# Kernel tuning notes

Hardware: AMD Instinct MI355X
Metric: run time of the kernel (lower is better)

The kernel has to match this reference:

```python
import jax, jax.numpy as jnp
import numpy as np

B, C, S, NSEG = 8, 64, 64, 256   # batch, channels, spatial, superpixel classes
DIM, DEPTH, HEADS, DH, MLP, NCLS = 256, 4, 8, 64, 1024, 4
D2 = 2 * DIM                      # transformer width = 512
INNER = HEADS * DH                # 512


def layernorm(x, g, b, eps=1e-5):
    mu = jnp.mean(x, axis=-1, keepdims=True)
    var = jnp.var(x, axis=-1, keepdims=True)
    return (x - mu) * jax.lax.rsqrt(var + eps) * g + b


def setup_inputs() -> dict:
    key = jax.random.key(0)
    ks = jax.random.split(key, 16)
    inp = {
        "image": jax.random.normal(ks[0], (B, 3, S, S), jnp.float32),
        "feature": jax.random.normal(ks[1], (3, B, C, S, S), jnp.float32),
        "superpixel": jax.random.randint(ks[2], (B, S, S), 0, NSEG),
        # patch embedding Linear(64*64*64 -> dim)
        "W_patch": jax.random.normal(ks[3], (C * S * S, DIM), jnp.float32) * (C * S * S) ** -0.5,
        "b_patch": jnp.zeros((DIM,), jnp.float32),
        # per-layer stacked params (depth leading axis)
        "ln1_g": jnp.ones((DEPTH, D2), jnp.float32),
        "ln1_b": jnp.zeros((DEPTH, D2), jnp.float32),
        "Wqkv": jax.random.normal(ks[4], (DEPTH, D2, 3 * INNER), jnp.float32) * D2 ** -0.5,
        "Wo": jax.random.normal(ks[5], (DEPTH, INNER, D2), jnp.float32) * INNER ** -0.5,
        "bo": jnp.zeros((DEPTH, D2), jnp.float32),
        "ln2_g": jnp.ones((DEPTH, D2), jnp.float32),
        "ln2_b": jnp.zeros((DEPTH, D2), jnp.float32),
        "W1": jax.random.normal(ks[6], (DEPTH, D2, MLP), jnp.float32) * D2 ** -0.5,
        "b1": jnp.zeros((DEPTH, MLP), jnp.float32),
        "W2": jax.random.normal(ks[7], (DEPTH, MLP, D2), jnp.float32) * MLP ** -0.5,
        "b2": jnp.zeros((DEPTH, D2), jnp.float32),
        # mlp_head: LayerNorm(2*dim) + Linear(2*dim, num_classes)
        "lnf_g": jnp.ones((D2,), jnp.float32),
        "lnf_b": jnp.zeros((D2,), jnp.float32),
        "W_head": jax.random.normal(ks[8], (D2, NCLS), jnp.float32) * D2 ** -0.5,
        "b_head": jnp.zeros((NCLS,), jnp.float32),
    }
    return inp


def _forward(image, feature, superpixel,
             W_patch, b_patch,
             ln1_g, ln1_b, Wqkv, Wo, bo, ln2_g, ln2_b, W1, b1, W2, b2,
             lnf_g, lnf_b, W_head, b_head):
    feat2 = feature[2]                                   # [B,C,S,S]
    # Fuse (one-hot mask * feature) -> flatten(b j h) -> Linear into a
    # per-pixel projection followed by a segment-sum over superpixel ids.
    Wr = W_patch.reshape(C, S, S, DIM)                   # matches (b j h) flatten order
    T = jnp.einsum('ibjh,bjhd->ijhd', feat2, Wr)         # [B,S,S,DIM]
    onehot = jax.nn.one_hot(superpixel, NSEG, dtype=T.dtype)  # [B,S,S,NSEG]
    x = jnp.einsum('ijha,ijhd->iad', onehot, T) + b_patch     # [B,NSEG,DIM]

    local = x
    g = jnp.max(x, axis=1, keepdims=True)                # global max over patches
    x = jnp.concatenate([jnp.broadcast_to(g, local.shape), local], axis=2)  # [B,256,2*dim]

    scale = DH ** -0.5
    for d in range(DEPTH):
        # attention block (pre-norm, residual)
        h = layernorm(x, ln1_g[d], ln1_b[d])
        qkv = h @ Wqkv[d]                                # [B,N,3*inner]
        q, k, v = jnp.split(qkv, 3, axis=-1)
        q = q.reshape(*q.shape[:2], HEADS, DH).transpose(0, 2, 1, 3)
        k = k.reshape(*k.shape[:2], HEADS, DH).transpose(0, 2, 1, 3)
        v = v.reshape(*v.shape[:2], HEADS, DH).transpose(0, 2, 1, 3)
        dots = jnp.einsum('bhnd,bhmd->bhnm', q, k) * scale
        attn = jax.nn.softmax(dots, axis=-1)
        o = jnp.einsum('bhnm,bhmd->bhnd', attn, v)
        o = o.transpose(0, 2, 1, 3).reshape(*x.shape[:2], INNER)
        x = x + (o @ Wo[d] + bo[d])
        # feedforward block (GELU exact, as nn.GELU default)
        h = layernorm(x, ln2_g[d], ln2_b[d])
        h = jax.nn.gelu(h @ W1[d] + b1[d], approximate=False)
        x = x + (h @ W2[d] + b2[d])

    return layernorm(x, lnf_g, lnf_b) @ W_head + b_head  # [B,256,num_classes]


def reference(image, feature, superpixel,
              W_patch, b_patch,
              ln1_g, ln1_b, Wqkv, Wo, bo, ln2_g, ln2_b, W1, b1, W2, b2,
              lnf_g, lnf_b, W_head, b_head):
    return _forward(image, feature, superpixel,
                    W_patch, b_patch,
                    ln1_g, ln1_b, Wqkv, Wo, bo, ln2_g, ln2_b, W1, b1, W2, b2,
                    lnf_g, lnf_b, W_head, b_head)
```

## Files before the change

### kernel.cpp

```cpp
#include <hip/hip_runtime.h>
#include <hip/hip_bf16.h>
#include <math.h>

#define NB 8
#define NC 64
#define NS 64
#define NPIX 4096
#define NSEG 256
#define DIM 256
#define DEPTH 4
#define HEADS 8
#define DHD 64
#define MLPD 1024
#define NCLS 4
#define D2 512
#define INNER 512
#define NTOK 2048

typedef unsigned short u16;
typedef unsigned int u32;
typedef __attribute__((ext_vector_type(4))) float f32x4;
typedef __attribute__((ext_vector_type(8))) short short8;

__device__ __forceinline__ u16 bf16_rne(float x) {
    u32 u = __float_as_uint(x);
    return (u16)((u + 0x7FFFu + ((u >> 16) & 1u)) >> 16);
}
__device__ __forceinline__ void split2(float x, u16& h, u16& l) {
    h = bf16_rne(x);
    float hf = __uint_as_float((u32)h << 16);
    l = bf16_rne(x - hf);
}

__global__ __launch_bounds__(256) void k_init_x0(float* __restrict__ x0,
                                                 const float* __restrict__ bp) {
    int idx = blockIdx.x * 256 + threadIdx.x;
    x0[idx] = bp[idx & (DIM - 1)];
}

#define PPB 4
__global__ __launch_bounds__(256) void k_patch(const float* __restrict__ feature,
                                               const int* __restrict__ sp,
                                               const float* __restrict__ Wp,
                                               float* __restrict__ x0) {
    __shared__ __align__(16) float f[NB * NC][PPB];
    __shared__ int seg[NB][PPB];
    const int p0 = blockIdx.x * PPB;
    const int t = threadIdx.x;
    const float* feat2 = feature + (size_t)2 * NB * NC * NPIX;
    #pragma unroll
    for (int i = 0; i < 2; ++i) {
        int pair = t + i * 256;
        *(float4*)&f[pair][0] = *(const float4*)&feat2[(size_t)pair * NPIX + p0];
    }
    if (t < NB * PPB) seg[t >> 2][t & 3] = sp[(t >> 2) * NPIX + p0 + (t & 3)];
    __syncthreads();
    const int d = t;
    for (int q = 0; q < PPB; ++q) {
        float acc[NB];
        #pragma unroll
        for (int b = 0; b < NB; ++b) acc[b] = 0.f;
        const float* wcol = Wp + (size_t)(p0 + q) * DIM + d;
        #pragma unroll 8
        for (int c = 0; c < NC; ++c) {
            float w = wcol[(size_t)c * NPIX * DIM];
            #pragma unroll
            for (int b = 0; b < NB; ++b) acc[b] = fmaf(f[b * NC + c][q], w, acc[b]);
        }
        #pragma unroll
        for (int b = 0; b < NB; ++b)
            atomicAdd(&x0[((b * NSEG) + seg[b][q]) * DIM + d], acc[b]);
    }
}

__global__ __launch_bounds__(256) void k_concat(const float* __restrict__ x0,
                                                float* __restrict__ x) {
    const int b = blockIdx.x, part = blockIdx.y;
    const int d = threadIdx.x;
    const float* xb = x0 + (size_t)b * NSEG * DIM;
    float g = -INFINITY;
    for (int s = 0; s < NSEG; ++s) g = fmaxf(g, xb[s * DIM + d]);
    for (int s = part * 16; s < part * 16 + 16; ++s) {
        float* row = x + ((size_t)(b * NSEG + s)) * D2;
        row[d] = g;
        row[DIM + d] = xb[s * DIM + d];
    }
}

__global__ __launch_bounds__(128) void k_ln(const float* __restrict__ x,
                                            const float* __restrict__ g,
                                            const float* __restrict__ bta,
                                            u16* __restrict__ outH,
                                            u16* __restrict__ outL) {
    const int row = blockIdx.x, t = threadIdx.x;
    const float4 v = *(const float4*)(x + (size_t)row * D2 + t * 4);
    float s = v.x + v.y + v.z + v.w;
    float ss = v.x * v.x + v.y * v.y + v.z * v.z + v.w * v.w;
    #pragma unroll
    for (int o = 32; o; o >>= 1) { s += __shfl_down(s, o); ss += __shfl_down(ss, o); }
    __shared__ float red[4];
    if ((t & 63) == 0) { red[(t >> 6) * 2] = s; red[(t >> 6) * 2 + 1] = ss; }
    __syncthreads();
    s = red[0] + red[2]; ss = red[1] + red[3];
    const float mu = s * (1.f / D2);
    const float rstd = rsqrtf(ss * (1.f / D2) - mu * mu + 1e-5f);
    const float4 g4 = *(const float4*)(g + t * 4);
    const float4 b4 = *(const float4*)(bta + t * 4);
    float o4[4] = {(v.x - mu) * rstd * g4.x + b4.x,
                   (v.y - mu) * rstd * g4.y + b4.y,
                   (v.z - mu) * rstd * g4.z + b4.z,
                   (v.w - mu) * rstd * g4.w + b4.w};
    u16 h[4], l[4];
    #pragma unroll
    for (int i = 0; i < 4; ++i) split2(o4[i], h[i], l[i]);
    *(ushort4*)(outH + (size_t)row * D2 + t * 4) = make_ushort4(h[0], h[1], h[2], h[3]);
    *(ushort4*)(outL + (size_t)row * D2 + t * 4) = make_ushort4(l[0], l[1], l[2], l[3]);
}

__device__ __forceinline__ void cvt_tile(const float* __restrict__ src, int K, int N,
                                         u16* __restrict__ dH, u16* __restrict__ dL,
                                         int k0, int n0) {
    __shared__ __align__(16) float ls[32][33];
    const int t = threadIdx.x;
    const int r = t >> 3, cg = t & 7;
    const float4 v = *(const float4*)(src + (size_t)(k0 + r) * N + n0 + cg * 4);
    ls[r][cg * 4 + 0] = v.x; ls[r][cg * 4 + 1] = v.y;
    ls[r][cg * 4 + 2] = v.z; ls[r][cg * 4 + 3] = v.w;
    __syncthreads();
    u16 h[4], l[4];
    #pragma unroll
    for (int i = 0; i < 4; ++i) split2(ls[cg * 4 + i][r], h[i], l[i]);
    *(ushort4*)(dH + (size_t)(n0 + r) * K + k0 + cg * 4) = make_ushort4(h[0], h[1], h[2], h[3]);
    *(ushort4*)(dL + (size_t)(n0 + r) * K + k0 + cg * 4) = make_ushort4(l[0], l[1], l[2], l[3]);
}

__global__ __launch_bounds__(256) void k_cvtT(const float* __restrict__ src,
                                              u16* __restrict__ dH, u16* __restrict__ dL,
                                              int K, int N) {
    cvt_tile(src, K, N, dH, dL, blockIdx.x * 32, blockIdx.y * 32);
}

__global__ __launch_bounds__(256) void k_cvtT3(const float* __restrict__ sO,
                                               const float* __restrict__ s1,
                                               const float* __restrict__ s2,
                                               u16* __restrict__ wb) {
    int K, N; const float* src; u16 *dH, *dL;
    if (blockIdx.z == 0)      { K = 512;  N = 512;  src = sO; dH = wb;           dL = wb + 262144; }
    else if (blockIdx.z == 1) { K = 512;  N = 1024; src = s1; dH = wb + 524288;  dL = wb + 1048576; }
    else                      { K = 1024; N = 512;  src = s2; dH = wb + 1572864; dL = wb + 2097152; }
    const int k0 = blockIdx.x * 32, n0 = blockIdx.y * 32;
    if (k0 >= K || n0 >= N) return;
    cvt_tile(src, K, N, dH, dL, k0, n0);
}

template<int K, int NN, int MODE>
__global__ __launch_bounds__(256) void k_mfmm(const u16* __restrict__ Ah,
                                              const u16* __restrict__ Al,
                                              const u16* __restrict__ Bh,
                                              const u16* __restrict__ Bl,
                                              const float* __restrict__ bias,
                                              float* __restrict__ Cf,
                                              u16* __restrict__ CoH,
                                              u16* __restrict__ CoL) {
    __shared__ __align__(16) u16 AsH[128][40], AsL[128][40], BsH[128][40], BsL[128][40];
    const int m0 = blockIdx.x * 128, n0 = blockIdx.y * 128;
    const int t = threadIdx.x;
    const int srow = t >> 1, soff = (t & 1) * 16;
    const int lane = t & 63;
    const int wr = (t >> 7) & 1, wc = (t >> 6) & 1;
    const int lrow = lane & 15, lk = lane >> 4;

    const u16* pAh = Ah + (size_t)(m0 + srow) * K + soff;
    const u16* pAl = Al + (size_t)(m0 + srow) * K + soff;
    const u16* pBh = Bh + (size_t)(n0 + srow) * K + soff;
    const u16* pBl = Bl + (size_t)(n0 + srow) * K + soff;

    uint4 rAh0 = *(const uint4*)pAh,       rAh1 = *(const uint4*)(pAh + 8);
    uint4 rAl0 = *(const uint4*)pAl,       rAl1 = *(const uint4*)(pAl + 8);
    uint4 rBh0 = *(const uint4*)pBh,       rBh1 = *(const uint4*)(pBh + 8);
    uint4 rBl0 = *(const uint4*)pBl,       rBl1 = *(const uint4*)(pBl + 8);

    f32x4 acc[4][4];
    #pragma unroll
    for (int i = 0; i < 4; ++i)
        #pragma unroll
        for (int j = 0; j < 4; ++j) acc[i][j] = (f32x4){0.f, 0.f, 0.f, 0.f};

    #pragma unroll 1
    for (int k0 = 0; k0 < K; k0 += 32) {
        __syncthreads();
        *(uint4*)&AsH[srow][soff] = rAh0;  *(uint4*)&AsH[srow][soff + 8] = rAh1;
        *(uint4*)&AsL[srow][soff] = rAl0;  *(uint4*)&AsL[srow][soff + 8] = rAl1;
        *(uint4*)&BsH[srow][soff] = rBh0;  *(uint4*)&BsH[srow][soff + 8] = rBh1;
        *(uint4*)&BsL[srow][soff] = rBl0;  *(uint4*)&BsL[srow][soff + 8] = rBl1;
        __syncthreads();
        if (k0 + 32 < K) {
            rAh0 = *(const uint4*)(pAh + k0 + 32);  rAh1 = *(const uint4*)(pAh + k0 + 40);
            rAl0 = *(const uint4*)(pAl + k0 + 32);  rAl1 = *(const uint4*)(pAl + k0 + 40);
            rBh0 = *(const uint4*)(pBh + k0 + 32);  rBh1 = *(const uint4*)(pBh + k0 + 40);
            rBl0 = *(const uint4*)(pBl + k0 + 32);  rBl1 = *(const uint4*)(pBl + k0 + 40);
        }
        short8 ah[4], al[4], bh[4], bl[4];
        #pragma unroll
        for (int i = 0; i < 4; ++i) {
            ah[i] = *(const short8*)&AsH[wr * 64 + i * 16 + lrow][lk * 8];
            al[i] = *(const short8*)&AsL[wr * 64 + i * 16 + lrow][lk * 8];
            bh[i] = *(const short8*)&BsH[wc * 64 + i * 16 + lrow][lk * 8];
            bl[i] = *(const short8*)&BsL[wc * 64 + i * 16 + lrow][lk * 8];
        }
        #pragma unroll
        for (int i = 0; i < 4; ++i)
            #pragma unroll
            for (int j = 0; j < 4; ++j) {
                acc[i][j] = __builtin_amdgcn_mfma_f32_16x16x32_bf16(ah[i], bh[j], acc[i][j], 0, 0, 0);
                acc[i][j] = __builtin_amdgcn_mfma_f32_16x16x32_bf16(ah[i], bl[j], acc[i][j], 0, 0, 0);
                acc[i][j] = __builtin_amdgcn_mfma_f32_16x16x32_bf16(al[i], bh[j], acc[i][j], 0, 0, 0);
            }
    }
    #pragma unroll
    for (int i = 0; i < 4; ++i) {
        #pragma unroll
        for (int j = 0; j < 4; ++j) {
            #pragma unroll
            for (int r = 0; r < 4; ++r) {
                const int row = m0 + wr * 64 + i * 16 + lk * 4 + r;
                const int col = n0 + wc * 64 + j * 16 + lrow;
                float v = acc[i][j][r];
                if (MODE == 0) {
                    const int which = col >> 9, hd = (col >> 6) & 7, dh = col & 63;
                    const int b = row >> 8, nn = row & 255;
                    Cf[(size_t)which * (NB * HEADS * NSEG * DHD) +
                       ((size_t)(b * HEADS + hd) * NSEG + nn) * DHD + dh] = v;
                } else if (MODE == 1) {
                    float* xp = Cf + (size_t)row * NN + col;
                    *xp += v + bias[col];
                } else {
                    v += bias[col];
                    float gl = 0.5f * v * (1.f + erff(v * 0.70710678118654752f));
                    u16 h, l; split2(gl, h, l);
                    CoH[(size_t)row * NN + col] = h;
                    CoL[(size_t)row * NN + col] = l;
                }
            }
        }
    }
}

__device__ __forceinline__ void gemm_tile(const float* __restrict__ A, int lda,
                                          const float* __restrict__ Bm, int ldb,
                                          int K, float acc[4][4],
                                          float (*As)[68], float (*Bs)[64]) {
    const int t = threadIdx.x;
    const int arow = t >> 2, akg = t & 3;
    const int bk = t >> 4, bng = t & 15;
    const int tx = t & 15, ty = t >> 4;
    for (int k0 = 0; k0 < K; k0 += 16) {
        const float4 av = *(const float4*)(A + (size_t)arow * lda + k0 + akg * 4);
        const float4 bv = *(const float4*)(Bm + (size_t)(k0 + bk) * ldb + bng * 4);
        __syncthreads();
        As[akg * 4 + 0][arow] = av.x;
        As[akg * 4 + 1][arow] = av.y;
        As[akg * 4 + 2][arow] = av.z;
        As[akg * 4 + 3][arow] = av.w;
        *(float4*)(&Bs[bk][bng * 4]) = bv;
        __syncthreads();
        #pragma unroll
        for (int u = 0; u < 16; ++u) {
            const float4 a4 = *(const float4*)(&As[u][ty * 4]);
            const float4 b4 = *(const float4*)(&Bs[u][tx * 4]);
            const float a[4] = {a4.x, a4.y, a4.z, a4.w};
            const float b[4] = {b4.x, b4.y, b4.z, b4.w};
            #pragma unroll
            for (int i = 0; i < 4; ++i)
                #pragma unroll
                for (int j = 0; j < 4; ++j)
                    acc[i][j] = fmaf(a[i], b[j], acc[i][j]);
        }
    }
}

__global__ __launch_bounds__(256) void k_qk(const float* __restrict__ q,
                                            const float* __restrict__ kmat,
                                            float* __restrict__ sc) {
    __shared__ __align__(16) float Qs[16][68], Ks[16][68];
    const int bh = blockIdx.z;
    const int t = threadIdx.x;
    const int arow = t >> 2, akg = t & 3, tx = t & 15, ty = t >> 4;
    const float* qb = q + ((size_t)bh * NSEG + blockIdx.x * 64) * DHD;
    const float* kb = kmat + ((size_t)bh * NSEG + blockIdx.y * 64) * DHD;
    float acc[4][4] = {};
    for (int k0 = 0; k0 < DHD; k0 += 16) {
        const float4 qv = *(const float4*)(qb + arow * DHD + k0 + akg * 4);
        const float4 kv = *(const float4*)(kb + arow * DHD + k0 + akg * 4);
        __syncthreads();
        Qs[akg * 4 + 0][arow] = qv.x; Qs[akg * 4 + 1][arow] = qv.y;
        Qs[akg * 4 + 2][arow] = qv.z; Qs[akg * 4 + 3][arow] = qv.w;
        Ks[akg * 4 + 0][arow] = kv.x; Ks[akg * 4 + 1][arow] = kv.y;
        Ks[akg * 4 + 2][arow] = kv.z; Ks[akg * 4 + 3][arow] = kv.w;
        __syncthreads();
        #pragma unroll
        for (int u = 0; u < 16; ++u) {
            const float4 a4 = *(const float4*)(&Qs[u][ty * 4]);
            const float4 b4 = *(const float4*)(&Ks[u][tx * 4]);
            const float a[4] = {a4.x, a4.y, a4.z, a4.w};
            const float b[4] = {b4.x, b4.y, b4.z, b4.w};
            #pragma unroll
            for (int i = 0; i < 4; ++i)
                #pragma unroll
                for (int j = 0; j < 4; ++j)
                    acc[i][j] = fmaf(a[i], b[j], acc[i][j]);
        }
    }
    float* sb = sc + (size_t)bh * NSEG * NSEG + (size_t)(blockIdx.x * 64) * NSEG + blockIdx.y * 64;
    #pragma unroll
    for (int i = 0; i < 4; ++i) {
        float4 o4 = make_float4(acc[i][0] * 0.125f, acc[i][1] * 0.125f,
                                acc[i][2] * 0.125f, acc[i][3] * 0.125f);
        *(float4*)(sb + (size_t)(ty * 4 + i) * NSEG + tx * 4) = o4;
    }
}

__global__ __launch_bounds__(256) void k_softmax(float* __restrict__ sc) {
    const int row = blockIdx.x * 4 + (threadIdx.x >> 6);
    const int l = threadIdx.x & 63;
    float* p = sc + (size_t)row * 256 + l * 4;
    float4 v = *(float4*)p;
    float m = fmaxf(fmaxf(v.x, v.y), fmaxf(v.z, v.w));
    #pragma unroll
    for (int o = 32; o; o >>= 1) m = fmaxf(m, __shfl_xor(m, o));
    v.x = __expf(v.x - m); v.y = __expf(v.y - m);
    v.z = __expf(v.z - m); v.w = __expf(v.w - m);
    float s = v.x + v.y + v.z + v.w;
    #pragma unroll
    for (int o = 32; o; o >>= 1) s += __shfl_xor(s, o);
    const float r = 1.f / s;
    v.x *= r; v.y *= r; v.z *= r; v.w *= r;
    *(float4*)p = v;
}

__global__ __launch_bounds__(256) void k_pv(const float* __restrict__ sc,
                                            const float* __restrict__ vmat,
                                            u16* __restrict__ oH,
                                            u16* __restrict__ oL) {
    __shared__ __align__(16) float As[16][68], Bs[16][64];
    const int bh = blockIdx.z;
    const int m0 = blockIdx.x * 64;
    float acc[4][4] = {};
    gemm_tile(sc + (size_t)bh * NSEG * NSEG + (size_t)m0 * NSEG, NSEG,
              vmat + (size_t)bh * NSEG * DHD, DHD, NSEG, acc, As, Bs);
    const int t = threadIdx.x, tx = t & 15, ty = t >> 4;
    #pragma unroll
    for (int i = 0; i < 4; ++i) {
        const size_t idx = (size_t)(bh >> 3) * NSEG * INNER + (bh & 7) * DHD +
                           (size_t)(m0 + ty * 4 + i) * INNER + tx * 4;
        u16 h[4], l[4];
        #pragma unroll
        for (int j = 0; j < 4; ++j) split2(acc[i][j], h[j], l[j]);
        *(ushort4*)(oH + idx) = make_ushort4(h[0], h[1], h[2], h[3]);
        *(ushort4*)(oL + idx) = make_ushort4(l[0], l[1], l[2], l[3]);
    }
}

__global__ __launch_bounds__(128) void k_head(const float* __restrict__ x,
                                              const float* __restrict__ g,
                                              const float* __restrict__ bta,
                                              const float* __restrict__ Wh,
                                              const float* __restrict__ bhd,
                                              float* __restrict__ out) {
    const int row = blockIdx.x, t = threadIdx.x;
    const float4 v = *(const float4*)(x + (size_t)row * D2 + t * 4);
    float s = v.x + v.y + v.z + v.w;
    float ss = v.x * v.x + v.y * v.y + v.z * v.z + v.w * v.w;
    #pragma unroll
    for (int o = 32; o; o >>= 1) { s += __shfl_down(s, o); ss += __shfl_down(ss, o); }
    __shared__ float red[4];
    if ((t & 63) == 0) { red[(t >> 6) * 2] = s; red[(t >> 6) * 2 + 1] = ss; }
    __syncthreads();
    s = red[0] + red[2]; ss = red[1] + red[3];
    const float mu = s * (1.f / D2);
    const float rstd = rsqrtf(ss * (1.f / D2) - mu * mu + 1e-5f);
    const float4 g4 = *(const float4*)(g + t * 4);
    const float4 b4 = *(const float4*)(bta + t * 4);
    const float hv[4] = {(v.x - mu) * rstd * g4.x + b4.x,
                         (v.y - mu) * rstd * g4.y + b4.y,
                         (v.z - mu) * rstd * g4.z + b4.z,
                         (v.w - mu) * rstd * g4.w + b4.w};
    float p[4] = {0, 0, 0, 0};
    #pragma unroll
    for (int i = 0; i < 4; ++i) {
        const float4 w = *(const float4*)(Wh + (size_t)(t * 4 + i) * NCLS);
        p[0] = fmaf(hv[i], w.x, p[0]); p[1] = fmaf(hv[i], w.y, p[1]);
        p[2] = fmaf(hv[i], w.z, p[2]); p[3] = fmaf(hv[i], w.w, p[3]);
    }
    #pragma unroll
    for (int o = 32; o; o >>= 1)
        #pragma unroll
        for (int c2 = 0; c2 < 4; ++c2) p[c2] += __shfl_down(p[c2], o);
    __shared__ float red2[2][4];
    if ((t & 63) == 0) {
        #pragma unroll
        for (int c2 = 0; c2 < 4; ++c2) red2[t >> 6][c2] = p[c2];
    }
    __syncthreads();
    if (t < 4) out[(size_t)row * NCLS + t] = red2[0][t] + red2[1][t] + bhd[t];
}

extern "C" void kernel_launch(void* const* d_in, const int* in_sizes, int n_in,
                              void* d_out, int out_size, void* d_ws, size_t ws_size,
                              hipStream_t stream) {
    const float* feature = (const float*)d_in[1];
    const int*   sp      = (const int*)d_in[2];
    const float* Wp      = (const float*)d_in[3];
    const float* bp      = (const float*)d_in[4];
    const float* ln1g    = (const float*)d_in[5];
    const float* ln1b    = (const float*)d_in[6];
    const float* Wqkv    = (const float*)d_in[7];
    const float* Wo      = (const float*)d_in[8];
    const float* bo      = (const float*)d_in[9];
    const float* ln2g    = (const float*)d_in[10];
    const float* ln2b    = (const float*)d_in[11];
    const float* W1      = (const float*)d_in[12];
    const float* b1      = (const float*)d_in[13];
    const float* W2      = (const float*)d_in[14];
    const float* b2      = (const float*)d_in[15];
    const float* lnfg    = (const float*)d_in[16];
    const float* lnfb    = (const float*)d_in[17];
    const float* Wh      = (const float*)d_in[18];
    const float* bhd     = (const float*)d_in[19];
    float* out = (float*)d_out;
    float* ws  = (float*)d_ws;

    float* x    = ws;
    float* x0   = ws + 1048576;
    u16*   hlnH = (u16*)(ws + 1572864);
    u16*   hlnL = hlnH + 1048576;
    u16*   h1H  = (u16*)(ws + 2621440);
    u16*   h1L  = h1H + 2097152;
    float* qkv  = ws + 4718592;
    float* sc   = ws + 7864320;
    u16*   wbuf = (u16*)sc;
    u16*   oH   = (u16*)(ws + 12058624);
    u16*   oL   = oH + 1048576;

    u16* qh = wbuf;
    u16* ql = wbuf + 786432;
    u16* woh = wbuf;
    u16* wol = wbuf + 262144;
    u16* w1h = wbuf + 524288;
    u16* w1l = wbuf + 1048576;
    u16* w2h = wbuf + 1572864;
    u16* w2l = wbuf + 2097152;

    k_init_x0<<<2048, 256, 0, stream>>>(x0, bp);
    k_patch<<<NPIX / PPB, 256, 0, stream>>>(feature, sp, Wp, x0);
    k_concat<<<dim3(NB, 16), 256, 0, stream>>>(x0, x);

    for (int d = 0; d < DEPTH; ++d) {
        k_cvtT<<<dim3(16, 48), 256, 0, stream>>>(Wqkv + (size_t)d * D2 * 3 * INNER,
                                                 qh, ql, D2, 3 * INNER);
        k_ln<<<NTOK, 128, 0, stream>>>(x, ln1g + d * D2, ln1b + d * D2, hlnH, hlnL);
        k_mfmm<512, 1536, 0><<<dim3(16, 12), 256, 0, stream>>>(
            hlnH, hlnL, qh, ql, nullptr, qkv, nullptr, nullptr);
        k_qk<<<dim3(4, 4, 64), 256, 0, stream>>>(qkv, qkv + 1048576, sc);
        k_softmax<<<4096, 256, 0, stream>>>(sc);
        k_pv<<<dim3(4, 1, 64), 256, 0, stream>>>(sc, qkv + 2097152, oH, oL);
        k_cvtT3<<<dim3(32, 32, 3), 256, 0, stream>>>(Wo + (size_t)d * INNER * D2,
                                                     W1 + (size_t)d * D2 * MLPD,
                                                     W2 + (size_t)d * MLPD * D2, wbuf);
        k_mfmm<512, 512, 1><<<dim3(16, 4), 256, 0, stream>>>(
            oH, oL, woh, wol, bo + d * D2, x, nullptr, nullptr);
        k_ln<<<NTOK, 128, 0, stream>>>(x, ln2g + d * D2, ln2b + d * D2, hlnH, hlnL);
        k_mfmm<512, 1024, 2><<<dim3(16, 8), 256, 0, stream>>>(
            hlnH, hlnL, w1h, w1l, b1 + d * MLPD, nullptr, h1H, h1L);
        k_mfmm<1024, 512, 1><<<dim3(16, 4), 256, 0, stream>>>(
            h1H, h1L, w2h, w2l, b2 + d * D2, x, nullptr, nullptr);
    }
    k_head<<<NTOK, 128, 0, stream>>>(x, lnfg, lnfb, Wh, bhd, out);
}
```

Measured before the change: 1.103 ms.

## Fuse attention QK, softmax and PV into one MFMA kernel with split-bf16 QKV

Replaces the three fp32 SIMT attention kernels (QK scores, softmax, PV) with a single fused kernel using bf16x3 split MFMA. The QKV projection epilogue now writes hi/lo bf16 halves directly, with V stored transposed for the PV MFMA operand. Scores stay in registers, and probabilities pass through per-wave LDS, so the 256x256 score matrix no longer round-trips through global memory. The cost is heavy register pressure (16 score accumulators) and scattered 2-byte global stores in the QKV epilogue.

Result: no change. 1.098 ms (-0.5%).

```diff
diff --git a/kernel.cpp b/kernel.cpp
--- a/kernel.cpp
+++ b/kernel.cpp
@@ -229,8 +229,13 @@
                 if (MODE == 0) {
                     const int which = col >> 9, hd = (col >> 6) & 7, dh = col & 63;
                     const int b = row >> 8, nn = row & 255;
-                    Cf[(size_t)which * (NB * HEADS * NSEG * DHD) +
-                       ((size_t)(b * HEADS + hd) * NSEG + nn) * DHD + dh] = v;
+                    u16 h, l; split2(v, h, l);
+                    size_t off;
+                    if (which == 2)
+                        off = (size_t)4194304 + ((size_t)((b * 8 + hd) * 64 + dh)) * 256 + nn;
+                    else
+                        off = (size_t)which * 2097152 + ((size_t)((b * 8 + hd) * 256 + nn)) * 64 + dh;
+                    CoH[off] = h; CoH[off + 1048576] = l;
                 } else if (MODE == 1) {
                     float* xp = Cf + (size_t)row * NN + col;
                     *xp += v + bias[col];
@@ -246,118 +251,106 @@
     }
 }
 
-__device__ __forceinline__ void gemm_tile(const float* __restrict__ A, int lda,
-                                          const float* __restrict__ Bm, int ldb,
-                                          int K, float acc[4][4],
-                                          float (*As)[68], float (*Bs)[64]) {
-    const int t = threadIdx.x;
-    const int arow = t >> 2, akg = t & 3;
-    const int bk = t >> 4, bng = t & 15;
-    const int tx = t & 15, ty = t >> 4;
-    for (int k0 = 0; k0 < K; k0 += 16) {
-        const float4 av = *(const float4*)(A + (size_t)arow * lda + k0 + akg * 4);
-        const float4 bv = *(const float4*)(Bm + (size_t)(k0 + bk) * ldb + bng * 4);
-        __syncthreads();
-        As[akg * 4 + 0][arow] = av.x;
-        As[akg * 4 + 1][arow] = av.y;
-        As[akg * 4 + 2][arow] = av.z;
-        As[akg * 4 + 3][arow] = av.w;
-        *(float4*)(&Bs[bk][bng * 4]) = bv;
-        __syncthreads();
-        #pragma unroll
-        for (int u = 0; u < 16; ++u) {
-            const float4 a4 = *(const float4*)(&As[u][ty * 4]);
-            const float4 b4 = *(const float4*)(&Bs[u][tx * 4]);
-            const float a[4] = {a4.x, a4.y, a4.z, a4.w};
-            const float b[4] = {b4.x, b4.y, b4.z, b4.w};
-            #pragma unroll
-            for (int i = 0; i < 4; ++i)
-                #pragma unroll
-                for (int j = 0; j < 4; ++j)
-                    acc[i][j] = fmaf(a[i], b[j], acc[i][j]);
-        }
-    }
-}
-
-__global__ __launch_bounds__(256) void k_qk(const float* __restrict__ q,
-                                            const float* __restrict__ kmat,
-                                            float* __restrict__ sc) {
-    __shared__ __align__(16) float Qs[16][68], Ks[16][68];
-    const int bh = blockIdx.z;
-    const int t = threadIdx.x;
-    const int arow = t >> 2, akg = t & 3, tx = t & 15, ty = t >> 4;
-    const float* qb = q + ((size_t)bh * NSEG + blockIdx.x * 64) * DHD;
-    const float* kb = kmat + ((size_t)bh * NSEG + blockIdx.y * 64) * DHD;
-    float acc[4][4] = {};
-    for (int k0 = 0; k0 < DHD; k0 += 16) {
-        const float4 qv = *(const float4*)(qb + arow * DHD + k0 + akg * 4);
-        const float4 kv = *(const float4*)(kb + arow * DHD + k0 + akg * 4);
-        __syncthreads();
-        Qs[akg * 4 + 0][arow] = qv.x; Qs[akg * 4 + 1][arow] = qv.y;
-        Qs[akg * 4 + 2][arow] = qv.z; Qs[akg * 4 + 3][arow] = qv.w;
-        Ks[akg * 4 + 0][arow] = kv.x; Ks[akg * 4 + 1][arow] = kv.y;
-        Ks[akg * 4 + 2][arow] = kv.z; Ks[akg * 4 + 3][arow] = kv.w;
-        __syncthreads();
-        #pragma unroll
-        for (int u = 0; u < 16; ++u) {
-            const float4 a4 = *(const float4*)(&Qs[u][ty * 4]);
-            const float4 b4 = *(const float4*)(&Ks[u][tx * 4]);
-            const float a[4] = {a4.x, a4.y, a4.z, a4.w};
-            const float b[4] = {b4.x, b4.y, b4.z, b4.w};
-            #pragma unroll
-            for (int i = 0; i < 4; ++i)
-                #pragma unroll
-                for (int j = 0; j < 4; ++j)
-                    acc[i][j] = fmaf(a[i], b[j], acc[i][j]);
-        }
-    }
-    float* sb = sc + (size_t)bh * NSEG * NSEG + (size_t)(blockIdx.x * 64) * NSEG + blockIdx.y * 64;
-    #pragma unroll
-    for (int i = 0; i < 4; ++i) {
-        float4 o4 = make_float4(acc[i][0] * 0.125f, acc[i][1] * 0.125f,
-                                acc[i][2] * 0.125f, acc[i][3] * 0.125f);
-        *(float4*)(sb + (size_t)(ty * 4 + i) * NSEG + tx * 4) = o4;
-    }
-}
-
-__global__ __launch_bounds__(256) void k_softmax(float* __restrict__ sc) {
-    const int row = blockIdx.x * 4 + (threadIdx.x >> 6);
-    const int l = threadIdx.x & 63;
-    float* p = sc + (size_t)row * 256 + l * 4;
-    float4 v = *(float4*)p;
-    float m = fmaxf(fmaxf(v.x, v.y), fmaxf(v.z, v.w));
-    #pragma unroll
-    for (int o = 32; o; o >>= 1) m = fmaxf(m, __shfl_xor(m, o));
-    v.x = __expf(v.x - m); v.y = __expf(v.y - m);
-    v.z = __expf(v.z - m); v.w = __expf(v.w - m);
-    float s = v.x + v.y + v.z + v.w;
-    #pragma unroll
-    for (int o = 32; o; o >>= 1) s += __shfl_xor(s, o);
-    const float r = 1.f / s;
-    v.x *= r; v.y *= r; v.z *= r; v.w *= r;
-    *(float4*)p = v;
-}
-
-__global__ __launch_bounds__(256) void k_pv(const float* __restrict__ sc,
-                                            const float* __restrict__ vmat,
-                                            u16* __restrict__ oH,
-                                            u16* __restrict__ oL) {
-    __shared__ __align__(16) float As[16][68], Bs[16][64];
-    const int bh = blockIdx.z;
-    const int m0 = blockIdx.x * 64;
-    float acc[4][4] = {};
-    gemm_tile(sc + (size_t)bh * NSEG * NSEG + (size_t)m0 * NSEG, NSEG,
-              vmat + (size_t)bh * NSEG * DHD, DHD, NSEG, acc, As, Bs);
-    const int t = threadIdx.x, tx = t & 15, ty = t >> 4;
-    #pragma unroll
-    for (int i = 0; i < 4; ++i) {
-        const size_t idx = (size_t)(bh >> 3) * NSEG * INNER + (bh & 7) * DHD +
-                           (size_t)(m0 + ty * 4 + i) * INNER + tx * 4;
-        u16 h[4], l[4];
-        #pragma unroll
-        for (int j = 0; j < 4; ++j) split2(acc[i][j], h[j], l[j]);
-        *(ushort4*)(oH + idx) = make_ushort4(h[0], h[1], h[2], h[3]);
-        *(ushort4*)(oL + idx) = make_ushort4(l[0], l[1], l[2], l[3]);
+__global__ __launch_bounds__(256) void k_attn(const u16* __restrict__ qkvS,
+                                              u16* __restrict__ oH,
+                                              u16* __restrict__ oL) {
+    __shared__ __align__(16) u16 Ph[4][16][264], Pl[4][16][264];
+    const int bh = blockIdx.y;
+    const int w = threadIdx.x >> 6, lane = threadIdx.x & 63;
+    const int row = lane & 15, hi = lane >> 4;
+    const int r0 = blockIdx.x * 64 + w * 16;
+
+    const u16* qHp = qkvS;
+    const u16* qLp = qkvS + 1048576;
+    const u16* kHp = qkvS + 2097152;
+    const u16* kLp = qkvS + 3145728;
+    const u16* vHp = qkvS + 4194304;
+    const u16* vLp = qkvS + 5242880;
+
+    short8 qh[2], ql[2];
+    #pragma unroll
+    for (int ks = 0; ks < 2; ++ks) {
+        const size_t a = ((size_t)bh * 256 + r0 + row) * 64 + ks * 32 + hi * 8;
+        qh[ks] = *(const short8*)(qHp + a);
+        ql[ks] = *(const short8*)(qLp + a);
+    }
+
+    f32x4 sacc[16];
+    #pragma unroll
+    for (int j = 0; j < 16; ++j) sacc[j] = (f32x4){0.f, 0.f, 0.f, 0.f};
+    #pragma unroll
+    for (int j = 0; j < 16; ++j) {
+        #pragma unroll
+        for (int ks = 0; ks < 2; ++ks) {
+            const size_t a = ((size_t)bh * 256 + j * 16 + row) * 64 + ks * 32 + hi * 8;
+            short8 kh = *(const short8*)(kHp + a);
+            short8 kl = *(const short8*)(kLp + a);
+            sacc[j] = __builtin_amdgcn_mfma_f32_16x16x32_bf16(qh[ks], kh, sacc[j], 0, 0, 0);
+            sacc[j] = __builtin_amdgcn_mfma_f32_16x16x32_bf16(qh[ks], kl, sacc[j], 0, 0, 0);
+            sacc[j] = __builtin_amdgcn_mfma_f32_16x16x32_bf16(ql[ks], kh, sacc[j], 0, 0, 0);
+        }
+    }
+
+    float rsum[4];
+    #pragma unroll
+    for (int r = 0; r < 4; ++r) {
+        float m = sacc[0][r];
+        #pragma unroll
+        for (int j = 1; j < 16; ++j) m = fmaxf(m, sacc[j][r]);
+        #pragma unroll
+        for (int o = 1; o < 16; o <<= 1) m = fmaxf(m, __shfl_xor(m, o));
+        float s = 0.f;
+        #pragma unroll
+        for (int j = 0; j < 16; ++j) {
+            float e = __expf((sacc[j][r] - m) * 0.125f);
+            sacc[j][r] = e;
+            s += e;
+        }
+        #pragma unroll
+        for (int o = 1; o < 16; o <<= 1) s += __shfl_xor(s, o);
+        rsum[r] = 1.f / s;
+    }
+
+    #pragma unroll
+    for (int j = 0; j < 16; ++j) {
+        #pragma unroll
+        for (int r = 0; r < 4; ++r) {
+            u16 h, l; split2(sacc[j][r], h, l);
+            Ph[w][4 * hi + r][row + 16 * j] = h;
+            Pl[w][4 * hi + r][row + 16 * j] = l;
+        }
+    }
+    __syncthreads();
+
+    f32x4 oacc[4];
+    #pragma unroll
+    for (int df = 0; df < 4; ++df) oacc[df] = (f32x4){0.f, 0.f, 0.f, 0.f};
+    #pragma unroll
+    for (int ks = 0; ks < 8; ++ks) {
+        short8 pah = *(const short8*)&Ph[w][row][ks * 32 + hi * 8];
+        short8 pal = *(const short8*)&Pl[w][row][ks * 32 + hi * 8];
+        #pragma unroll
+        for (int df = 0; df < 4; ++df) {
+            const size_t a = ((size_t)bh * 64 + df * 16 + row) * 256 + ks * 32 + hi * 8;
+            short8 vh = *(const short8*)(vHp + a);
+            short8 vl = *(const short8*)(vLp + a);
+            oacc[df] = __builtin_amdgcn_mfma_f32_16x16x32_bf16(pah, vh, oacc[df], 0, 0, 0);
+            oacc[df] = __builtin_amdgcn_mfma_f32_16x16x32_bf16(pah, vl, oacc[df], 0, 0, 0);
+            oacc[df] = __builtin_amdgcn_mfma_f32_16x16x32_bf16(pal, vh, oacc[df], 0, 0, 0);
+        }
+    }
+
+    const int b = bh >> 3, hd = bh & 7;
+    #pragma unroll
+    for (int df = 0; df < 4; ++df) {
+        #pragma unroll
+        for (int r = 0; r < 4; ++r) {
+            float v = oacc[df][r] * rsum[r];
+            u16 h, l; split2(v, h, l);
+            const int n = r0 + 4 * hi + r;
+            const size_t idx = ((size_t)(b * 256 + n)) * 512 + hd * 64 + df * 16 + row;
+            oH[idx] = h; oL[idx] = l;
+        }
     }
 }
 
@@ -436,7 +429,7 @@
     u16*   hlnL = hlnH + 1048576;
     u16*   h1H  = (u16*)(ws + 2621440);
     u16*   h1L  = h1H + 2097152;
-    float* qkv  = ws + 4718592;
+    u16*   qkvS = (u16*)(ws + 4718592);
     float* sc   = ws + 7864320;
     u16*   wbuf = (u16*)sc;
     u16*   oH   = (u16*)(ws + 12058624);
@@ -460,10 +453,8 @@
                                                  qh, ql, D2, 3 * INNER);
         k_ln<<<NTOK, 128, 0, stream>>>(x, ln1g + d * D2, ln1b + d * D2, hlnH, hlnL);
         k_mfmm<512, 1536, 0><<<dim3(16, 12), 256, 0, stream>>>(
-            hlnH, hlnL, qh, ql, nullptr, qkv, nullptr, nullptr);
-        k_qk<<<dim3(4, 4, 64), 256, 0, stream>>>(qkv, qkv + 1048576, sc);
-        k_softmax<<<4096, 256, 0, stream>>>(sc);
-        k_pv<<<dim3(4, 1, 64), 256, 0, stream>>>(sc, qkv + 2097152, oH, oL);
+            hlnH, hlnL, qh, ql, nullptr, nullptr, qkvS, nullptr);
+        k_attn<<<dim3(4, 64), 256, 0, stream>>>(qkvS, oH, oL);
         k_cvtT3<<<dim3(32, 32, 3), 256, 0, stream>>>(Wo + (size_t)d * INNER * D2,
                                                      W1 + (size_t)d * D2 * MLPD,
                                                      W2 + (size_t)d * MLPD * D2, wbuf);
```
